# Kernel optimization log

Measured on AMD Instinct MI355X. Metric: run time of the kernel, lower is better.

## Reference

```python
import jax, jax.numpy as jnp
import numpy as np

HIDDEN = 128
N_RBF = 32
LMAX = 2
N_NODES = 10000
DEG = 8  # each node has DEG outgoing (and DEG incoming) edges on a ring


def _build_graph():
    src = np.repeat(np.arange(N_NODES, dtype=np.int64), DEG)
    offs = np.tile(np.arange(1, DEG + 1, dtype=np.int64), N_NODES)
    dst = (src + offs) % N_NODES
    keys = src * N_NODES + dst
    order = np.argsort(keys)
    src2, dst2 = src[order], dst[order]  # e2 sorted by key (searchsorted invariant)
    e1_to_e2 = np.empty_like(order)
    e1_to_e2[order] = np.arange(order.size)
    return src, dst, src2, dst2, e1_to_e2


def setup_inputs() -> dict:
    key = jax.random.key(0)
    ks = jax.random.split(key, 12)
    src1, dst1, src2, dst2, e1_to_e2 = _build_graph()
    E1, E2 = src1.size, src2.size
    in_dim = 6 * HIDDEN + 3 * N_RBF + 1  # 865

    def lin(k, fi, fo):
        kw, kb = jax.random.split(k)
        s = 1.0 / np.sqrt(fi)
        return (jax.random.uniform(kw, (fi, fo), minval=-s, maxval=s),
                jax.random.uniform(kb, (fo,), minval=-s, maxval=s))

    w1, b1 = lin(ks[0], in_dim, HIDDEN)
    w2, b2 = lin(ks[1], HIDDEN, HIDDEN)
    wgw, bgw = lin(ks[2], HIDDEN, HIDDEN)
    wgt, bgt = lin(ks[3], HIDDEN, HIDDEN)
    return {
        "t_e2": jax.random.normal(ks[4], (E2, HIDDEN), dtype=jnp.float32),
        "h": jax.random.normal(ks[5], (N_NODES, HIDDEN), dtype=jnp.float32),
        "edge_index1": jnp.asarray(np.stack([src1, dst1])),
        "edge_index2": jnp.asarray(np.stack([src2, dst2])),
        "e1_to_e2": jnp.asarray(e1_to_e2),
        "dist_e1": jax.random.uniform(ks[6], (E1,), dtype=jnp.float32),
        "dist_e2": jax.random.uniform(ks[7], (E2,), dtype=jnp.float32),
        "rbf_e1": jax.random.normal(ks[8], (E1, N_RBF), dtype=jnp.float32),
        "rbf_e2": jax.random.normal(ks[9], (E2, N_RBF), dtype=jnp.float32),
        "sph_e1": jax.random.normal(ks[10], (E1, LMAX + 1), dtype=jnp.float32),
        "num_nodes": N_NODES,
        "w1": w1, "b1": b1, "w2": w2, "b2": b2,
        "wgw": wgw, "bgw": bgw, "wgt": wgt, "bgt": bgt,
    }


def _wedge_indices(edge_index1, edge_index2, num_nodes):
    """Host-side (numpy, vectorized) wedge construction: for every center node k,
    all (incoming edge i->k, outgoing edge k->j) pairs with i != j, kept only when
    (i, j) itself is an edge in e2 (looked up by sorted key search)."""
    src1 = np.asarray(edge_index1[0]); dst1 = np.asarray(edge_index1[1])
    src2 = np.asarray(edge_index2[0]); dst2 = np.asarray(edge_index2[1])
    nz = src1 != dst1  # drop self-loops
    s, d = src1[nz], dst1[nz]
    eid = np.nonzero(nz)[0]
    out_deg = np.bincount(s, minlength=num_nodes)
    out_order = np.argsort(s, kind="stable")  # filtered-edge positions grouped by src
    out_ptr = np.concatenate([np.zeros(1, np.int64), np.cumsum(out_deg)])
    reps = out_deg[d]  # each incoming edge pairs with out_deg[center] outgoing edges
    total = int(reps.sum())
    if total == 0:
        z = np.zeros(0, np.int64)
        return z, z, z, z, z, z
    starts = np.cumsum(reps) - reps
    local = np.arange(total) - np.repeat(starts, reps)
    kj_f = out_order[np.repeat(out_ptr[d], reps) + local]
    i = np.repeat(s, reps)
    k = np.repeat(d, reps)
    eik = np.repeat(eid, reps)
    j = d[kj_f]
    ekj = eid[kj_f]
    m = i != j
    i, k, j, eik, ekj = i[m], k[m], j[m], eik[m], ekj[m]
    e2_keys = src2.astype(np.int64) * num_nodes + dst2
    pk = i.astype(np.int64) * num_nodes + j
    pos = np.searchsorted(e2_keys, pk)
    posc = np.minimum(pos, e2_keys.size - 1)
    valid = (pos < e2_keys.size) & (e2_keys[posc] == pk)
    return i[valid], k[valid], j[valid], eik[valid], ekj[valid], posc[valid]


def reference(t_e2, h, edge_index1, edge_index2, e1_to_e2, dist_e1, dist_e2,
              rbf_e1, rbf_e2, sph_e1, num_nodes,
              w1, b1, w2, b2, wgw, bgw, wgt, bgt):
    i, k, j, eik, ekj, eij = _wedge_indices(edge_index1, edge_index2, int(num_nodes))
    if i.size == 0:
        return t_e2
    i, k, j = jnp.asarray(i), jnp.asarray(k), jnp.asarray(j)
    eik, ekj, eij = jnp.asarray(eik), jnp.asarray(ekj), jnp.asarray(eij)
    e1e2 = jnp.asarray(e1_to_e2)
    # wedge geometric features (wedge_use_high_degree=False -> l=1 contraction only)
    c_feat = (sph_e1[eik, 1] * sph_e1[ekj, 1])[:, None]           # [W, 1]
    g = jnp.concatenate([rbf_e1[eik], rbf_e1[ekj], rbf_e2[eij], c_feat], axis=-1)
    rho_in = jnp.concatenate([t_e2[e1e2[eik]], t_e2[e1e2[ekj]], t_e2[eij],
                              h[i], h[k], h[j], g], axis=-1)       # [W, 865]
    msg = jax.nn.silu(rho_in @ w1 + b1) @ w2 + b2                  # [W, H]
    m = jax.ops.segment_sum(msg, eij, num_segments=t_e2.shape[0])  # [E2, H]
    return t_e2 + jax.nn.sigmoid(m @ wgw + bgw) * jnp.tanh(t_e2 @ wgt + bgt)
```

## Files before the change

kernel.cpp:

```cpp
#include <hip/hip_runtime.h>
#include <math.h>

typedef unsigned short u16;
typedef unsigned int u32;
typedef __bf16 bf16x8 __attribute__((ext_vector_type(8)));
typedef float f32x4 __attribute__((ext_vector_type(4)));

__device__ __forceinline__ float bf2f(u16 v){ union{u32 u;float f;}c; c.u=((u32)v)<<16; return c.f; }
__device__ __forceinline__ u16 f2bf(float f){ union{float f;u32 u;}c; c.f=f; u32 l=(c.u>>16)&1u; c.u+=0x7fffu+l; return (u16)(c.u>>16); }
__device__ __forceinline__ u32 pk2(float a, float b){ return (u32)f2bf(a) | ((u32)f2bf(b)<<16); }
__device__ __forceinline__ uint4 ld8f(const float* p){
  float4 x = ((const float4*)p)[0];
  float4 y = ((const float4*)p)[1];
  uint4 r; r.x=pk2(x.x,x.y); r.y=pk2(x.z,x.w); r.z=pk2(y.x,y.y); r.w=pk2(y.z,y.w);
  return r;
}
__device__ __forceinline__ float fsilu(float x){ return x/(1.f+__expf(-x)); }


__global__ void k_setup_edges(const int* __restrict__ e1_to_e2,
                              const float* __restrict__ rbf_e1,
                              const float* __restrict__ sph_e1,
                              u16* __restrict__ rbf1p,
                              float* __restrict__ sph_c, int E1) {
  int e = blockIdx.x*256 + threadIdx.x;
  if (e >= E1) return;
  int f = e1_to_e2[e];
  sph_c[f] = sph_e1[e*3+1];
  const float* s = rbf_e1 + (size_t)e*32;
  uint4* d = (uint4*)(rbf1p + (size_t)f*32);
  d[0]=ld8f(s); d[1]=ld8f(s+8); d[2]=ld8f(s+16); d[3]=ld8f(s+24);
}

__global__ void k_out_ptr(const int* __restrict__ src2, int* __restrict__ out_ptr,
                          int Nn, int E2) {
  int n = blockIdx.x*256 + threadIdx.x;
  if (n > Nn) return;
  int lo=0, hi=E2;
  while (lo<hi){ int m=(lo+hi)>>1; if (src2[m]<n) lo=m+1; else hi=m; }
  out_ptr[n]=lo;
}

__global__ void k_wbigt(const float* __restrict__ w1, u16* __restrict__ WbigT) {
  int id = blockIdx.x*256+threadIdx.x;
  if (id >= 384*448) return;
  int n = id/448, k = id%448;
  int q = n>>7, nn = n&127;
  int row = -1;
  if (k<128) row = q*128+k;
  else if (k<256) { if (q==0) row = 384+(k-128); }
  else if (k<384) { if (q==0) row = 512+(k-256); else if (q==1) row = 640+(k-256); }
  else if (k<416) { if (q==0) row = 768+(k-384); else if (q==1) row = 800+(k-384); }
  else { if (q==2) row = 832+(k-416); }
  WbigT[id] = (row>=0) ? f2bf(w1[row*128+nn]) : (u16)0;
}

__global__ void k_smallw(const float* __restrict__ w2, const float* __restrict__ wgw,
                         const float* __restrict__ wgt, const float* __restrict__ b2,
                         u16* __restrict__ WcT, u16* __restrict__ WgtT,
                         float* __restrict__ bc2) {
  int id = blockIdx.x*256+threadIdx.x;
  if (id < 16384) {
    int n = id&127, k = id>>7;
    float s = 0.f;
    for (int r=0;r<128;r++) s += w2[k*128+r]*wgw[r*128+n];
    WcT[n*128+k] = f2bf(s);
    WgtT[n*128+k] = f2bf(wgt[k*128+n]);
  } else if (id < 16384+128) {
    int n = id-16384;
    float s = 0.f;
    for (int r=0;r<128;r++) s += b2[r]*wgw[r*128+n];
    bc2[n] = s;
  }
}

__global__ __launch_bounds__(256, 8)
void k_enum(const int* __restrict__ src2, const int* __restrict__ dst2,
            const int* __restrict__ out_ptr, const float* __restrict__ sph_c,
            int4* __restrict__ wrec, int* __restrict__ cnt, int E2) {
  int id = blockIdx.x*256 + threadIdx.x;
  if (id >= E2*8) return;
  int gw = id >> 3, d = id & 7;
  int i = src2[gw], j = dst2[gw];
  int f = out_ptr[i] + d;
  if (f >= out_ptr[i+1]) return;
  int k = dst2[f];
  int lo = out_ptr[k], hi = out_ptr[k+1], hi0 = hi;
  while (lo<hi) { int m=(lo+hi)>>1; if (dst2[m]<j) lo=m+1; else hi=m; }
  if (lo < hi0 && dst2[lo]==j) {
    float cf = sph_c[f]*sph_c[lo];
    int slot = atomicAdd(&cnt[gw], 1);
    int4 r; r.x=f; r.y=lo; r.z=__float_as_int(cf); r.w=0;
    wrec[(size_t)gw*8 + slot] = r;
  }
}

__global__ __launch_bounds__(256, 8)
void k_wedge2(const u16* __restrict__ Q1, const u16* __restrict__ Q2,
              const u16* __restrict__ P3, const int4* __restrict__ wrec,
              const int* __restrict__ cnt, const float* __restrict__ w1,
              u16* __restrict__ S, int E2) {
  int gw = (int)((blockIdx.x*256 + threadIdx.x) >> 6);
  int lane = threadIdx.x & 63;
  if (gw >= E2) return;
  u32 p3u = ((const u32*)(P3 + (size_t)gw*128))[lane];
  float p30 = bf2f((u16)(p3u&0xffff)), p31 = bf2f((u16)(p3u>>16));
  float2 wv = ((const float2*)(w1 + 864*128))[lane];
  const u32* q1b = (const u32*)Q1;
  const u32* q2b = (const u32*)Q2;
  const int4* wr = wrec + (size_t)gw*8;
  int c = cnt[gw];
  float a0=0.f, a1=0.f;
  int w = 0;
  for (; w+2<=c; w+=2) {
    int4 rA = wr[w], rB = wr[w+1];
    u32 xA = q1b[(size_t)rA.x*64 + lane];
    u32 yA = q2b[(size_t)rA.y*64 + lane];
    u32 xB = q1b[(size_t)rB.x*64 + lane];
    u32 yB = q2b[(size_t)rB.y*64 + lane];
    float cfA = __int_as_float(rA.z), cfB = __int_as_float(rB.z);
    float x0 = p30 + bf2f((u16)(xA&0xffff)) + bf2f((u16)(yA&0xffff)) + cfA*wv.x;
    float x1 = p31 + bf2f((u16)(xA>>16))    + bf2f((u16)(yA>>16))    + cfA*wv.y;
    float z0 = p30 + bf2f((u16)(xB&0xffff)) + bf2f((u16)(yB&0xffff)) + cfB*wv.x;
    float z1 = p31 + bf2f((u16)(xB>>16))    + bf2f((u16)(yB>>16))    + cfB*wv.y;
    a0 += fsilu(x0) + fsilu(z0);
    a1 += fsilu(x1) + fsilu(z1);
  }
  if (w < c) {
    int4 rA = wr[w];
    u32 xA = q1b[(size_t)rA.x*64 + lane];
    u32 yA = q2b[(size_t)rA.y*64 + lane];
    float cfA = __int_as_float(rA.z);
    float x0 = p30 + bf2f((u16)(xA&0xffff)) + bf2f((u16)(yA&0xffff)) + cfA*wv.x;
    float x1 = p31 + bf2f((u16)(xA>>16))    + bf2f((u16)(yA>>16))    + cfA*wv.y;
    a0 += fsilu(x0);
    a1 += fsilu(x1);
  }
  ((u32*)(S + (size_t)gw*128))[lane] = pk2(a0, a1);
}

struct GArgs {
  const float* t_f32; const float* h; const float* rbf_e2;
  const u16* rbf1p; const u16* Asrc;
  const int* src2; const int* dst2; const int* cnt;
  const u16* Bmat; const u16* Gin;
  const float* b1; const float* bgw; const float* bgt; const float* bc2;
  u16* out0; u16* out1; u16* out2;
  float* outf;
  int M;
};

template<int MODE>
__global__ __launch_bounds__(256, 2)
void k_gemm(GArgs a) {
  constexpr int KT = (MODE==0)?448:128;
  constexpr int NK = KT/32;
  __shared__ u16 As[128*40];
  __shared__ u16 Bs[128*40];
  const int tid = threadIdx.x;
  const int bm = blockIdx.x, bn = blockIdx.y;
  const int lane = tid & 63, wave = tid >> 6;
  const int wm = wave >> 1, wn = wave & 1;
  const int quad = lane >> 4, l16 = lane & 15;

  const int part = tid & 3;
  const int ra = tid >> 2;
  const int rb = ra + 64;
  long fa = (long)bm*128 + ra;
  long fb = (long)bm*128 + rb;
  if (fa >= a.M) fa = a.M-1;
  if (fb >= a.M) fb = a.M-1;
  int sa=0, da=0, sb=0, db=0;
  if constexpr (MODE==0) { sa=a.src2[fa]; da=a.dst2[fa]; sb=a.src2[fb]; db=a.dst2[fb]; }

  f32x4 acc[4][4] = {};
  for (int ks=0; ks<NK; ks++) {
    const int kb = ks*32;
    uint4 va, vb;
    if constexpr (MODE==0) {
      if (ks<4)       { va = ld8f(a.t_f32 + fa*128 + kb + part*8);
                        vb = ld8f(a.t_f32 + fb*128 + kb + part*8); }
      else if (ks<8)  { va = ld8f(a.h + (long)sa*128 + (kb-128) + part*8);
                        vb = ld8f(a.h + (long)sb*128 + (kb-128) + part*8); }
      else if (ks<12) { va = ld8f(a.h + (long)da*128 + (kb-256) + part*8);
                        vb = ld8f(a.h + (long)db*128 + (kb-256) + part*8); }
      else if (ks==12){ va = *(const uint4*)(a.rbf1p + fa*32 + part*8);
                        vb = *(const uint4*)(a.rbf1p + fb*32 + part*8); }
      else            { va = ld8f(a.rbf_e2 + fa*32 + part*8);
                        vb = ld8f(a.rbf_e2 + fb*32 + part*8); }
    } else if constexpr (MODE==1) {
      va = *(const uint4*)(a.Asrc + fa*128 + kb + part*8);
      vb = *(const uint4*)(a.Asrc + fb*128 + kb + part*8);
    } else {
      va = ld8f(a.t_f32 + fa*128 + kb + part*8);
      vb = ld8f(a.t_f32 + fb*128 + kb + part*8);
    }
    uint4 wa = *(const uint4*)(a.Bmat + (long)(bn*128 + ra)*KT + kb + part*8);
    uint4 wb = *(const uint4*)(a.Bmat + (long)(bn*128 + rb)*KT + kb + part*8);
    __syncthreads();
    *(uint4*)(As + ra*40 + part*8) = va;
    *(uint4*)(As + rb*40 + part*8) = vb;
    *(uint4*)(Bs + ra*40 + part*8) = wa;
    *(uint4*)(Bs + rb*40 + part*8) = wb;
    __syncthreads();
    bf16x8 af[4], bfr[4];
    #pragma unroll
    for (int t=0;t<4;t++) {
      af[t]  = *(const bf16x8*)(As + (wm*64 + t*16 + l16)*40 + quad*8);
      bfr[t] = *(const bf16x8*)(Bs + (wn*64 + t*16 + l16)*40 + quad*8);
    }
    #pragma unroll
    for (int tm=0;tm<4;tm++)
      #pragma unroll
      for (int tn=0;tn<4;tn++)
        acc[tm][tn] = __builtin_amdgcn_mfma_f32_16x16x32_bf16(af[tm], bfr[tn], acc[tm][tn], 0,0,0);
  }

  #pragma unroll
  for (int tm=0;tm<4;tm++) {
    const int rloc = wm*64 + tm*16 + quad*4;
    #pragma unroll
    for (int r=0;r<4;r++) {
      long row = (long)bm*128 + rloc + r;
      if (row >= a.M) continue;
      #pragma unroll
      for (int tn=0;tn<4;tn++) {
        const int col = wn*64 + tn*16 + l16;
        float v = acc[tm][tn][r];
        if constexpr (MODE==0) {
          u16* dst = (bn==0)? a.out0 : (bn==1)? a.out1 : a.out2;
          if (bn==2) v += a.b1[col];
          dst[row*128 + col] = f2bf(v);
        } else if constexpr (MODE==1) {
          float u = v + (float)a.cnt[row]*a.bc2[col] + a.bgw[col];
          float g = 1.f/(1.f+__expf(-u));
          a.out0[row*128+col] = f2bf(g);
        } else {
          float vv = v + a.bgt[col];
          float th = 1.f - 2.f/(__expf(2.f*vv)+1.f);
          float t  = a.t_f32[row*128+col];
          float g  = bf2f(a.Gin[row*128+col]);
          a.outf[row*128+col] = t + g*th;
        }
      }
    }
  }
}

extern "C" void kernel_launch(void* const* d_in, const int* in_sizes, int n_in,
                              void* d_out, int out_size, void* d_ws, size_t ws_size,
                              hipStream_t stream) {
  const float* t_e2  = (const float*)d_in[0];
  const float* h     = (const float*)d_in[1];
  const int* ei2     = (const int*)d_in[3];
  const int* e1_to_e2 = (const int*)d_in[4];
  const float* rbf_e1 = (const float*)d_in[7];
  const float* rbf_e2 = (const float*)d_in[8];
  const float* sph_e1 = (const float*)d_in[9];
  const float* w1  = (const float*)d_in[11];
  const float* b1  = (const float*)d_in[12];
  const float* w2  = (const float*)d_in[13];
  const float* b2  = (const float*)d_in[14];
  const float* wgw = (const float*)d_in[15];
  const float* bgw = (const float*)d_in[16];
  const float* wgt = (const float*)d_in[17];
  const float* bgt = (const float*)d_in[18];

  const int E2 = in_sizes[0]/128;
  const int Nn = in_sizes[1]/128;
  const int E1 = in_sizes[5];
  const int* src2 = ei2;
  const int* dst2 = ei2 + E2;

  char* p = (char*)d_ws;
  u16* Q1 = (u16*)p;       p += (size_t)E2*128*2;
  u16* Q2 = (u16*)p;       p += (size_t)E2*128*2;
  u16* P3 = (u16*)p;       p += (size_t)E2*128*2;
  u16* rbf1p = (u16*)p;    p += (size_t)E2*32*2;
  u16* WbigT = (u16*)p;    p += (size_t)384*448*2;
  u16* WcT   = (u16*)p;    p += (size_t)128*128*2;
  u16* WgtT  = (u16*)p;    p += (size_t)128*128*2;
  float* sph_c = (float*)p; p += (size_t)E2*4;
  float* bc2   = (float*)p; p += 512;
  int* out_ptr = (int*)p;   p += (((size_t)(Nn+1)*4 + 63)/64)*64;
  int* cnt     = (int*)p;   p += (size_t)E2*4;
  int4* wrec   = (int4*)p;  p += (size_t)E2*8*16;
  u16* S = P3;
  u16* G = Q1;

  hipMemsetAsync(cnt, 0, (size_t)E2*4, stream);

  k_setup_edges<<<(E1+255)/256, 256, 0, stream>>>(e1_to_e2, rbf_e1, sph_e1, rbf1p, sph_c, E1);
  k_out_ptr<<<(Nn+1+255)/256, 256, 0, stream>>>(src2, out_ptr, Nn, E2);
  k_wbigt<<<(384*448+255)/256, 256, 0, stream>>>(w1, WbigT);
  k_smallw<<<(16512+255)/256, 256, 0, stream>>>(w2, wgw, wgt, b2, WcT, WgtT, bc2);
  k_enum<<<(E2*8+255)/256, 256, 0, stream>>>(src2, dst2, out_ptr, sph_c, wrec, cnt, E2);

  const int Mb = (E2+127)/128;
  {
    GArgs a = {};
    a.t_f32=t_e2; a.h=h; a.rbf1p=rbf1p; a.rbf_e2=rbf_e2;
    a.src2=src2; a.dst2=dst2; a.Bmat=WbigT; a.b1=b1;
    a.out0=Q1; a.out1=Q2; a.out2=P3; a.M=E2;
    k_gemm<0><<<dim3(Mb,3), 256, 0, stream>>>(a);
  }
  k_wedge2<<<(E2+3)/4, 256, 0, stream>>>(Q1, Q2, P3, wrec, cnt, w1, S, E2);
  {
    GArgs a = {};
    a.Asrc=S; a.cnt=cnt; a.Bmat=WcT; a.bgw=bgw; a.bc2=bc2;
    a.out0=G; a.M=E2;
    k_gemm<1><<<dim3(Mb,1), 256, 0, stream>>>(a);
  }
  {
    GArgs a = {};
    a.t_f32=t_e2; a.Bmat=WgtT; a.bgt=bgt; a.Gin=G;
    a.outf=(float*)d_out; a.M=E2;
    k_gemm<2><<<dim3(Mb,1), 256, 0, stream>>>(a);
  }
}
```

Baseline: 337.4 us.

## Fuse three N-tiles of the wedge GEMM into one 512-thread double-buffered block

```diff
diff --git a/kernel.cpp b/kernel.cpp
--- a/kernel.cpp
+++ b/kernel.cpp
@@ -7,8 +7,10 @@
 typedef float f32x4 __attribute__((ext_vector_type(4)));
 
 __device__ __forceinline__ float bf2f(u16 v){ union{u32 u;float f;}c; c.u=((u32)v)<<16; return c.f; }
-__device__ __forceinline__ u16 f2bf(float f){ union{float f;u32 u;}c; c.f=f; u32 l=(c.u>>16)&1u; c.u+=0x7fffu+l; return (u16)(c.u>>16); }
-__device__ __forceinline__ u32 pk2(float a, float b){ return (u32)f2bf(a) | ((u32)f2bf(b)<<16); }
+__device__ __forceinline__ u16 f2bf(float f){ union{__bf16 h; u16 u;}c; c.h=(__bf16)f; return c.u; }
+__device__ __forceinline__ u32 pk2(float a, float b){
+  union{ __bf16 h[2]; u32 u; }c; c.h[0]=(__bf16)a; c.h[1]=(__bf16)b; return c.u;
+}
 __device__ __forceinline__ uint4 ld8f(const float* p){
   float4 x = ((const float4*)p)[0];
   float4 y = ((const float4*)p)[1];
@@ -150,10 +152,91 @@
   int M;
 };
 
+__device__ __forceinline__ uint4 loadA0(const GArgs& a, long fa, int sa, int da,
+                                        int part, int ks) {
+  const int kb = ks*32;
+  if (ks<4)   return ld8f(a.t_f32 + fa*128 + kb + part*8);
+  if (ks<8)   return ld8f(a.h + (long)sa*128 + (kb-128) + part*8);
+  if (ks<12)  return ld8f(a.h + (long)da*128 + (kb-256) + part*8);
+  if (ks==12) return *(const uint4*)(a.rbf1p + fa*32 + part*8);
+  return ld8f(a.rbf_e2 + fa*32 + part*8);
+}
+__device__ __forceinline__ void loadB0(const GArgs& a, int tid, int ks, uint4* wb) {
+  #pragma unroll
+  for (int s=0;s<3;s++){
+    int id = tid + s*512;
+    wb[s] = *(const uint4*)(a.Bmat + (long)(id>>2)*448 + ks*32 + (id&3)*8);
+  }
+}
+
+__global__ __launch_bounds__(512)
+void k_gemm0(GArgs a) {
+  __shared__ u16 As[2][128*40];
+  __shared__ u16 Bs[2][384*40];
+  const int tid = threadIdx.x;
+  const int bm = blockIdx.x;
+  const int lane = tid & 63, wave = tid >> 6;
+  const int wm = wave >> 2, wn = wave & 3;
+  const int quad = lane >> 4, l16 = lane & 15;
+
+  const int part = tid & 3;
+  const int ra = tid >> 2;
+  long fa = (long)bm*128 + ra;
+  if (fa >= a.M) fa = a.M-1;
+  const int sa = a.src2[fa], da = a.dst2[fa];
+
+  uint4 va = loadA0(a, fa, sa, da, part, 0);
+  uint4 wb[3]; loadB0(a, tid, 0, wb);
+
+  f32x4 acc[4][6] = {};
+  for (int ks=0; ks<14; ks++) {
+    const int cur = ks & 1;
+    *(uint4*)(As[cur] + ra*40 + part*8) = va;
+    #pragma unroll
+    for (int s=0;s<3;s++){
+      int id = tid + s*512;
+      *(uint4*)(Bs[cur] + (id>>2)*40 + (id&3)*8) = wb[s];
+    }
+    __syncthreads();
+    if (ks < 13) { va = loadA0(a, fa, sa, da, part, ks+1); loadB0(a, tid, ks+1, wb); }
+    bf16x8 af[4], bfr[6];
+    #pragma unroll
+    for (int t=0;t<4;t++)
+      af[t]  = *(const bf16x8*)(As[cur] + (wm*64 + t*16 + l16)*40 + quad*8);
+    #pragma unroll
+    for (int u=0;u<6;u++)
+      bfr[u] = *(const bf16x8*)(Bs[cur] + (wn*96 + u*16 + l16)*40 + quad*8);
+    #pragma unroll
+    for (int tm=0;tm<4;tm++)
+      #pragma unroll
+      for (int tn=0;tn<6;tn++)
+        acc[tm][tn] = __builtin_amdgcn_mfma_f32_16x16x32_bf16(af[tm], bfr[tn], acc[tm][tn], 0,0,0);
+  }
+
+  #pragma unroll
+  for (int tm=0;tm<4;tm++) {
+    const int rloc = wm*64 + tm*16 + quad*4;
+    #pragma unroll
+    for (int r=0;r<4;r++) {
+      long row = (long)bm*128 + rloc + r;
+      if (row >= a.M) continue;
+      #pragma unroll
+      for (int tn=0;tn<6;tn++) {
+        const int col = wn*96 + tn*16 + l16;
+        const int bn = col >> 7, cn = col & 127;
+        float v = acc[tm][tn][r];
+        if (bn==2) v += a.b1[cn];
+        u16* dst = (bn==0)? a.out0 : (bn==1)? a.out1 : a.out2;
+        dst[row*128 + cn] = f2bf(v);
+      }
+    }
+  }
+}
+
 template<int MODE>
 __global__ __launch_bounds__(256, 2)
 void k_gemm(GArgs a) {
-  constexpr int KT = (MODE==0)?448:128;
+  constexpr int KT = 128;
   constexpr int NK = KT/32;
   __shared__ u16 As[128*40];
   __shared__ u16 Bs[128*40];
@@ -170,25 +253,12 @@
   long fb = (long)bm*128 + rb;
   if (fa >= a.M) fa = a.M-1;
   if (fb >= a.M) fb = a.M-1;
-  int sa=0, da=0, sb=0, db=0;
-  if constexpr (MODE==0) { sa=a.src2[fa]; da=a.dst2[fa]; sb=a.src2[fb]; db=a.dst2[fb]; }
 
   f32x4 acc[4][4] = {};
   for (int ks=0; ks<NK; ks++) {
     const int kb = ks*32;
     uint4 va, vb;
-    if constexpr (MODE==0) {
-      if (ks<4)       { va = ld8f(a.t_f32 + fa*128 + kb + part*8);
-                        vb = ld8f(a.t_f32 + fb*128 + kb + part*8); }
-      else if (ks<8)  { va = ld8f(a.h + (long)sa*128 + (kb-128) + part*8);
-                        vb = ld8f(a.h + (long)sb*128 + (kb-128) + part*8); }
-      else if (ks<12) { va = ld8f(a.h + (long)da*128 + (kb-256) + part*8);
-                        vb = ld8f(a.h + (long)db*128 + (kb-256) + part*8); }
-      else if (ks==12){ va = *(const uint4*)(a.rbf1p + fa*32 + part*8);
-                        vb = *(const uint4*)(a.rbf1p + fb*32 + part*8); }
-      else            { va = ld8f(a.rbf_e2 + fa*32 + part*8);
-                        vb = ld8f(a.rbf_e2 + fb*32 + part*8); }
-    } else if constexpr (MODE==1) {
+    if constexpr (MODE==1) {
       va = *(const uint4*)(a.Asrc + fa*128 + kb + part*8);
       vb = *(const uint4*)(a.Asrc + fb*128 + kb + part*8);
     } else {
@@ -196,12 +266,12 @@
       vb = ld8f(a.t_f32 + fb*128 + kb + part*8);
     }
     uint4 wa = *(const uint4*)(a.Bmat + (long)(bn*128 + ra)*KT + kb + part*8);
-    uint4 wb = *(const uint4*)(a.Bmat + (long)(bn*128 + rb)*KT + kb + part*8);
+    uint4 wbv = *(const uint4*)(a.Bmat + (long)(bn*128 + rb)*KT + kb + part*8);
     __syncthreads();
     *(uint4*)(As + ra*40 + part*8) = va;
     *(uint4*)(As + rb*40 + part*8) = vb;
     *(uint4*)(Bs + ra*40 + part*8) = wa;
-    *(uint4*)(Bs + rb*40 + part*8) = wb;
+    *(uint4*)(Bs + rb*40 + part*8) = wbv;
     __syncthreads();
     bf16x8 af[4], bfr[4];
     #pragma unroll
@@ -227,11 +297,7 @@
       for (int tn=0;tn<4;tn++) {
         const int col = wn*64 + tn*16 + l16;
         float v = acc[tm][tn][r];
-        if constexpr (MODE==0) {
-          u16* dst = (bn==0)? a.out0 : (bn==1)? a.out1 : a.out2;
-          if (bn==2) v += a.b1[col];
-          dst[row*128 + col] = f2bf(v);
-        } else if constexpr (MODE==1) {
+        if constexpr (MODE==1) {
           float u = v + (float)a.cnt[row]*a.bc2[col] + a.bgw[col];
           float g = 1.f/(1.f+__expf(-u));
           a.out0[row*128+col] = f2bf(g);
@@ -302,7 +368,7 @@
     a.t_f32=t_e2; a.h=h; a.rbf1p=rbf1p; a.rbf_e2=rbf_e2;
     a.src2=src2; a.dst2=dst2; a.Bmat=WbigT; a.b1=b1;
     a.out0=Q1; a.out1=Q2; a.out2=P3; a.M=E2;
-    k_gemm<0><<<dim3(Mb,3), 256, 0, stream>>>(a);
+    k_gemm0<<<Mb, 512, 0, stream>>>(a);
   }
   k_wedge2<<<(E2+3)/4, 256, 0, stream>>>(Q1, Q2, P3, wrec, cnt, w1, S, E2);
   {
```

Result: slower. 410.4 us (+21.6%).
